# Kernel optimization log

Measured on AMD Instinct MI355X. Metric: run time of the kernel, lower is better.

The kernel has to match this reference:

```python
import jax, jax.numpy as jnp
import numpy as np

B, D, N, K = 16, 128, 16384, 64


def setup_inputs() -> dict:
    key = jax.random.key(0)
    k1, k2, k3, k4 = jax.random.split(key, 4)
    x = jax.random.normal(k1, (B, D, N), dtype=jnp.float32)
    mu = jax.random.normal(k2, (K, D), dtype=jnp.float32)
    log_sigma = 0.1 * jax.random.normal(k3, (K, D), dtype=jnp.float32)
    log_alpha = 0.1 * jax.random.normal(k4, (K,), dtype=jnp.float32)
    return {"x": x, "mu": mu, "log_sigma": log_sigma, "log_alpha": log_alpha}


def reference(x, mu, log_sigma, log_alpha):
    # x: (B, D, N) -> (B, N, D)
    xt = jnp.transpose(x, (0, 2, 1))
    # F.normalize(mu): L2-normalize each cluster center along D (eps=1e-12)
    mu_n = mu / jnp.maximum(jnp.linalg.norm(mu, axis=1, keepdims=True), 1e-12)
    sigma_inv = jnp.exp(-log_sigma)                     # (K, D)
    log_sigma_sum = jnp.sum(log_sigma, axis=1)          # (K,)
    # dist_{bnk} = sum_d (x-mu)^2 * sinv, decomposed into GEMMs
    xsq_term = jnp.einsum('bnd,kd->bnk', xt * xt, sigma_inv)
    cross = jnp.einsum('bnd,kd->bnk', xt, mu_n * sigma_inv)
    mu_term = jnp.sum(mu_n * mu_n * sigma_inv, axis=1)  # (K,)
    dist = xsq_term - 2.0 * cross + mu_term
    logits = -dist + log_alpha - 0.5 * log_sigma_sum    # (B, N, K)
    posterior = jax.nn.softmax(logits, axis=-1)
    return jnp.transpose(posterior, (0, 2, 1))          # (B, K, N)
```

## Files before the change

kernel.cpp:

```cpp
#include <hip/hip_runtime.h>

#define LOG2E 1.4426950408889634f

constexpr int Dn = 128;
constexpr int Nn = 16384;
constexpr int Kn = 64;
constexpr int Bn = 16;

typedef __attribute__((ext_vector_type(16))) float f32x16;

__global__ __launch_bounds__(64) void gmm_prep(const float* __restrict__ mu,
                                               const float* __restrict__ log_sigma,
                                               const float* __restrict__ log_alpha,
                                               float4* __restrict__ wout,
                                               float* __restrict__ cout) {
    const int k = blockIdx.x;
    const int l = threadIdx.x;
    const int d0 = 2 * l;
    float m0 = mu[k * Dn + d0];
    float m1 = mu[k * Dn + d0 + 1];
    float s0 = log_sigma[k * Dn + d0];
    float s1 = log_sigma[k * Dn + d0 + 1];
    float nrm2 = m0 * m0 + m1 * m1;
    float lss = s0 + s1;
    #pragma unroll
    for (int off = 32; off > 0; off >>= 1) {
        nrm2 += __shfl_xor(nrm2, off);
        lss  += __shfl_xor(lss, off);
    }
    const float inv_nrm = 1.0f / fmaxf(sqrtf(nrm2), 1e-12f);
    const float mn0 = m0 * inv_nrm, mn1 = m1 * inv_nrm;
    const float si0 = expf(-s0), si1 = expf(-s1);
    float mt = mn0 * mn0 * si0 + mn1 * mn1 * si1;
    #pragma unroll
    for (int off = 32; off > 0; off >>= 1) mt += __shfl_xor(mt, off);
    wout[((k >> 3) * 64 + l) * 8 + (k & 7)] =
        make_float4(-si0 * LOG2E, 2.0f * mn0 * si0 * LOG2E,
                    -si1 * LOG2E, 2.0f * mn1 * si1 * LOG2E);
    if (l == 0) cout[k] = (log_alpha[k] - 0.5f * lss - mt) * LOG2E;
}

__device__ __forceinline__ float4 fmax4(float4 a, float4 b) {
    return make_float4(fmaxf(a.x, b.x), fmaxf(a.y, b.y),
                       fmaxf(a.z, b.z), fmaxf(a.w, b.w));
}
__device__ __forceinline__ float4 add4(float4 a, float4 b) {
    return make_float4(a.x + b.x, a.y + b.y, a.z + b.z, a.w + b.w);
}

__global__ __launch_bounds__(512)
void gmm_main(const float* __restrict__ x,
              const float4* __restrict__ w,
              const float* __restrict__ cks,
              float* __restrict__ out) {
    __shared__ float sRed[8][256];

    const int tid = threadIdx.x;
    const int g = __builtin_amdgcn_readfirstlane(tid >> 6);
    const int l = tid & 63;
    const int b = blockIdx.y;
    const int nloc = 4 * l;
    const size_t nbase = (size_t)blockIdx.x * 256 + nloc;

    float acc[8][4];
    #pragma unroll
    for (int k = 0; k < 8; ++k) {
        const float c = cks[g * 8 + k];
        #pragma unroll
        for (int j = 0; j < 4; ++j) acc[k][j] = c;
    }

    const float* xp = x + (size_t)b * Dn * Nn + nbase;
    const char* wp = (const char*)w + (size_t)g * 8192;

    #pragma unroll 1
    for (int dh = 0; dh < Dn / 2; ++dh) {
        const float4 xa = *(const float4*)(xp);
        const float4 xb = *(const float4*)(xp + Nn);
        xp += 2 * Nn;

        f32x16 w0, w1;
        asm("s_load_dwordx16 %0, %2, 0x0\n\t"
            "s_load_dwordx16 %1, %2, 0x40\n\t"
            "s_waitcnt lgkmcnt(0)"
            : "=&s"(w0), "=&s"(w1)
            : "s"(wp));
        wp += 128;

        const float4 ta = make_float4(xa.x * xa.x, xa.y * xa.y,
                                      xa.z * xa.z, xa.w * xa.w);
        const float4 tb = make_float4(xb.x * xb.x, xb.y * xb.y,
                                      xb.z * xb.z, xb.w * xb.w);

#define GMM_K(WV, KK, A)                                                  \
        {                                                                 \
            const float wx0 = WV[4 * KK + 0], wy0 = WV[4 * KK + 1];       \
            const float wx1 = WV[4 * KK + 2], wy1 = WV[4 * KK + 3];       \
            A[0] = fmaf(wx0, ta.x, A[0]); A[0] = fmaf(wy0, xa.x, A[0]);   \
            A[0] = fmaf(wx1, tb.x, A[0]); A[0] = fmaf(wy1, xb.x, A[0]);   \
            A[1] = fmaf(wx0, ta.y, A[1]); A[1] = fmaf(wy0, xa.y, A[1]);   \
            A[1] = fmaf(wx1, tb.y, A[1]); A[1] = fmaf(wy1, xb.y, A[1]);   \
            A[2] = fmaf(wx0, ta.z, A[2]); A[2] = fmaf(wy0, xa.z, A[2]);   \
            A[2] = fmaf(wx1, tb.z, A[2]); A[2] = fmaf(wy1, xb.z, A[2]);   \
            A[3] = fmaf(wx0, ta.w, A[3]); A[3] = fmaf(wy0, xa.w, A[3]);   \
            A[3] = fmaf(wx1, tb.w, A[3]); A[3] = fmaf(wy1, xb.w, A[3]);   \
        }

        GMM_K(w0, 0, acc[0]); GMM_K(w0, 1, acc[1]);
        GMM_K(w0, 2, acc[2]); GMM_K(w0, 3, acc[3]);
        GMM_K(w1, 0, acc[4]); GMM_K(w1, 1, acc[5]);
        GMM_K(w1, 2, acc[6]); GMM_K(w1, 3, acc[7]);
#undef GMM_K
    }

    float4 m = make_float4(acc[0][0], acc[0][1], acc[0][2], acc[0][3]);
    #pragma unroll
    for (int k = 1; k < 8; ++k)
        m = fmax4(m, make_float4(acc[k][0], acc[k][1], acc[k][2], acc[k][3]));
    *(float4*)&sRed[g][nloc] = m;
    __syncthreads();
    #pragma unroll
    for (int gg = 0; gg < 8; ++gg)
        m = fmax4(m, *(const float4*)&sRed[gg][nloc]);
    __syncthreads();

    float4 s = make_float4(0.f, 0.f, 0.f, 0.f);
    #pragma unroll
    for (int k = 0; k < 8; ++k) {
        acc[k][0] = __builtin_amdgcn_exp2f(acc[k][0] - m.x); s.x += acc[k][0];
        acc[k][1] = __builtin_amdgcn_exp2f(acc[k][1] - m.y); s.y += acc[k][1];
        acc[k][2] = __builtin_amdgcn_exp2f(acc[k][2] - m.z); s.z += acc[k][2];
        acc[k][3] = __builtin_amdgcn_exp2f(acc[k][3] - m.w); s.w += acc[k][3];
    }
    *(float4*)&sRed[g][nloc] = s;
    __syncthreads();
    s = make_float4(0.f, 0.f, 0.f, 0.f);
    #pragma unroll
    for (int gg = 0; gg < 8; ++gg)
        s = add4(s, *(const float4*)&sRed[gg][nloc]);
    const float4 r = make_float4(1.0f / s.x, 1.0f / s.y, 1.0f / s.z, 1.0f / s.w);

    float* op = out + (size_t)(b * Kn + g * 8) * Nn + nbase;
    #pragma unroll
    for (int k = 0; k < 8; ++k) {
        *(float4*)op = make_float4(acc[k][0] * r.x, acc[k][1] * r.y,
                                   acc[k][2] * r.z, acc[k][3] * r.w);
        op += Nn;
    }
}

extern "C" void kernel_launch(void* const* d_in, const int* in_sizes, int n_in,
                              void* d_out, int out_size, void* d_ws, size_t ws_size,
                              hipStream_t stream) {
    const float* x  = (const float*)d_in[0];
    const float* mu = (const float*)d_in[1];
    const float* ls = (const float*)d_in[2];
    const float* la = (const float*)d_in[3];
    float* out = (float*)d_out;

    float4* wbuf = (float4*)d_ws;
    float*  cbuf = (float*)((char*)d_ws + (size_t)Kn * (Dn / 2) * sizeof(float4));

    gmm_prep<<<dim3(Kn), dim3(64), 0, stream>>>(mu, ls, la, wbuf, cbuf);
    gmm_main<<<dim3(Nn / 256, Bn), dim3(512), 0, stream>>>(x, wbuf, cbuf, out);
}
```

Measured before the change: 261.5 us.

## Compute GMM distance GEMMs with split-bf16 MFMA instead of scalar FMA

Replaces the per-thread FP32 FMA loop with v_mfma_f32_16x16x32_bf16. Weights and activations are split into hi/lo bf16 pairs to emulate near-FP32 accuracy, using three MFMAs per product term. The prep kernel now writes weights in MFMA fragment layout. The main kernel stages converted x tiles in LDS and uses smaller 64-column blocks with a cross-wave softmax reduction. The goal is to move the compute-bound inner product onto matrix cores, at the cost of bf16-split conversion work, scalar (non-vectorized) output stores and some accuracy risk.

```diff
diff --git a/kernel.cpp b/kernel.cpp
--- a/kernel.cpp
+++ b/kernel.cpp
@@ -7,12 +7,18 @@
 constexpr int Kn = 64;
 constexpr int Bn = 16;
 
-typedef __attribute__((ext_vector_type(16))) float f32x16;
+typedef float f32x4 __attribute__((ext_vector_type(4)));
+typedef unsigned int u32x4 __attribute__((ext_vector_type(4)));
+
+__device__ __forceinline__ unsigned int rnhi(float f) {
+    unsigned int u = __float_as_uint(f);
+    return (u + 0x7FFFu + ((u >> 16) & 1u)) & 0xFFFF0000u;
+}
 
 __global__ __launch_bounds__(64) void gmm_prep(const float* __restrict__ mu,
                                                const float* __restrict__ log_sigma,
                                                const float* __restrict__ log_alpha,
-                                               float4* __restrict__ wout,
+                                               unsigned short* __restrict__ wfrag,
                                                float* __restrict__ cout) {
     const int k = blockIdx.x;
     const int l = threadIdx.x;
@@ -34,118 +40,169 @@
     float mt = mn0 * mn0 * si0 + mn1 * mn1 * si1;
     #pragma unroll
     for (int off = 32; off > 0; off >>= 1) mt += __shfl_xor(mt, off);
-    wout[((k >> 3) * 64 + l) * 8 + (k & 7)] =
-        make_float4(-si0 * LOG2E, 2.0f * mn0 * si0 * LOG2E,
-                    -si1 * LOG2E, 2.0f * mn1 * si1 * LOG2E);
+
+    const float av[2] = {-si0 * LOG2E, -si1 * LOG2E};
+    const float bv[2] = {2.0f * mn0 * si0 * LOG2E, 2.0f * mn1 * si1 * LOG2E};
+    const int ks = k >> 4;
+    #pragma unroll
+    for (int dd = 0; dd < 2; ++dd) {
+        const int d = d0 + dd;
+        const unsigned int ah = rnhi(av[dd]);
+        const unsigned int al = rnhi(av[dd] - __uint_as_float(ah));
+        const unsigned int bh = rnhi(bv[dd]);
+        const unsigned int bl = rnhi(bv[dd] - __uint_as_float(bh));
+        const int s = d >> 5, h = (d >> 3) & 3, j = d & 7;
+        const int lane = (h << 4) | (k & 15);
+        const size_t base = ((size_t)((ks * 4 + s) * 4) * 64 + lane) * 8 + j;
+        wfrag[base + 0 * 64 * 8] = (unsigned short)(ah >> 16);
+        wfrag[base + 1 * 64 * 8] = (unsigned short)(al >> 16);
+        wfrag[base + 2 * 64 * 8] = (unsigned short)(bh >> 16);
+        wfrag[base + 3 * 64 * 8] = (unsigned short)(bl >> 16);
+    }
     if (l == 0) cout[k] = (log_alpha[k] - 0.5f * lss - mt) * LOG2E;
 }
 
-__device__ __forceinline__ float4 fmax4(float4 a, float4 b) {
-    return make_float4(fmaxf(a.x, b.x), fmaxf(a.y, b.y),
-                       fmaxf(a.z, b.z), fmaxf(a.w, b.w));
-}
-__device__ __forceinline__ float4 add4(float4 a, float4 b) {
-    return make_float4(a.x + b.x, a.y + b.y, a.z + b.z, a.w + b.w);
-}
-
 __global__ __launch_bounds__(512)
+__attribute__((amdgpu_waves_per_eu(4, 4)))
 void gmm_main(const float* __restrict__ x,
-              const float4* __restrict__ w,
+              const unsigned short* __restrict__ wf,
               const float* __restrict__ cks,
               float* __restrict__ out) {
-    __shared__ float sRed[8][256];
+    __shared__ unsigned short sB[4][4][4][64][8];
+    __shared__ float sRedM[4][64];
+    __shared__ float sRedS[4][64];
 
     const int tid = threadIdx.x;
-    const int g = __builtin_amdgcn_readfirstlane(tid >> 6);
     const int l = tid & 63;
     const int b = blockIdx.y;
-    const int nloc = 4 * l;
-    const size_t nbase = (size_t)blockIdx.x * 256 + nloc;
-
-    float acc[8][4];
-    #pragma unroll
-    for (int k = 0; k < 8; ++k) {
-        const float c = cks[g * 8 + k];
-        #pragma unroll
-        for (int j = 0; j < 4; ++j) acc[k][j] = c;
-    }
-
-    const float* xp = x + (size_t)b * Dn * Nn + nbase;
-    const char* wp = (const char*)w + (size_t)g * 8192;
-
-    #pragma unroll 1
-    for (int dh = 0; dh < Dn / 2; ++dh) {
-        const float4 xa = *(const float4*)(xp);
-        const float4 xb = *(const float4*)(xp + Nn);
-        xp += 2 * Nn;
-
-        f32x16 w0, w1;
-        asm("s_load_dwordx16 %0, %2, 0x0\n\t"
-            "s_load_dwordx16 %1, %2, 0x40\n\t"
-            "s_waitcnt lgkmcnt(0)"
-            : "=&s"(w0), "=&s"(w1)
-            : "s"(wp));
-        wp += 128;
-
-        const float4 ta = make_float4(xa.x * xa.x, xa.y * xa.y,
-                                      xa.z * xa.z, xa.w * xa.w);
-        const float4 tb = make_float4(xb.x * xb.x, xb.y * xb.y,
-                                      xb.z * xb.z, xb.w * xb.w);
-
-#define GMM_K(WV, KK, A)                                                  \
-        {                                                                 \
-            const float wx0 = WV[4 * KK + 0], wy0 = WV[4 * KK + 1];       \
-            const float wx1 = WV[4 * KK + 2], wy1 = WV[4 * KK + 3];       \
-            A[0] = fmaf(wx0, ta.x, A[0]); A[0] = fmaf(wy0, xa.x, A[0]);   \
-            A[0] = fmaf(wx1, tb.x, A[0]); A[0] = fmaf(wy1, xb.x, A[0]);   \
-            A[1] = fmaf(wx0, ta.y, A[1]); A[1] = fmaf(wy0, xa.y, A[1]);   \
-            A[1] = fmaf(wx1, tb.y, A[1]); A[1] = fmaf(wy1, xb.y, A[1]);   \
-            A[2] = fmaf(wx0, ta.z, A[2]); A[2] = fmaf(wy0, xa.z, A[2]);   \
-            A[2] = fmaf(wx1, tb.z, A[2]); A[2] = fmaf(wy1, xb.z, A[2]);   \
-            A[3] = fmaf(wx0, ta.w, A[3]); A[3] = fmaf(wy0, xa.w, A[3]);   \
-            A[3] = fmaf(wx1, tb.w, A[3]); A[3] = fmaf(wy1, xb.w, A[3]);   \
-        }
-
-        GMM_K(w0, 0, acc[0]); GMM_K(w0, 1, acc[1]);
-        GMM_K(w0, 2, acc[2]); GMM_K(w0, 3, acc[3]);
-        GMM_K(w1, 0, acc[4]); GMM_K(w1, 1, acc[5]);
-        GMM_K(w1, 2, acc[6]); GMM_K(w1, 3, acc[7]);
-#undef GMM_K
-    }
-
-    float4 m = make_float4(acc[0][0], acc[0][1], acc[0][2], acc[0][3]);
-    #pragma unroll
-    for (int k = 1; k < 8; ++k)
-        m = fmax4(m, make_float4(acc[k][0], acc[k][1], acc[k][2], acc[k][3]));
-    *(float4*)&sRed[g][nloc] = m;
+    const int nwin = blockIdx.x * 64;
+    const float* xwin = x + (size_t)b * Dn * Nn + nwin;
+
+    float xv[2][8];
+    #pragma unroll
+    for (int i = 0; i < 2; ++i) {
+        const int o = (tid >> 6) + 8 * i;
+        #pragma unroll
+        for (int jj = 0; jj < 8; ++jj)
+            xv[i][jj] = xwin[(size_t)(o * 8 + jj) * Nn + l];
+    }
+    #pragma unroll
+    for (int i = 0; i < 2; ++i) {
+        const int o = (tid >> 6) + 8 * i;
+        const int s = o >> 2, h = o & 3;
+        const int lane = (h << 4) | (l & 15), tt = l >> 4;
+        unsigned int XH[4], XL[4], TH[4], TL[4];
+        #pragma unroll
+        for (int p = 0; p < 4; ++p) {
+            const float x0 = xv[i][2 * p], x1 = xv[i][2 * p + 1];
+            const float t0 = x0 * x0, t1 = x1 * x1;
+            const unsigned int xh0 = rnhi(x0), xh1 = rnhi(x1);
+            const unsigned int xq0 = rnhi(x0 - __uint_as_float(xh0));
+            const unsigned int xq1 = rnhi(x1 - __uint_as_float(xh1));
+            const unsigned int th0 = rnhi(t0), th1 = rnhi(t1);
+            const unsigned int tq0 = rnhi(t0 - __uint_as_float(th0));
+            const unsigned int tq1 = rnhi(t1 - __uint_as_float(th1));
+            XH[p] = (xh0 >> 16) | xh1;
+            XL[p] = (xq0 >> 16) | xq1;
+            TH[p] = (th0 >> 16) | th1;
+            TL[p] = (tq0 >> 16) | tq1;
+        }
+        *(u32x4*)&sB[0][s][tt][lane][0] = u32x4{XH[0], XH[1], XH[2], XH[3]};
+        *(u32x4*)&sB[1][s][tt][lane][0] = u32x4{XL[0], XL[1], XL[2], XL[3]};
+        *(u32x4*)&sB[2][s][tt][lane][0] = u32x4{TH[0], TH[1], TH[2], TH[3]};
+        *(u32x4*)&sB[3][s][tt][lane][0] = u32x4{TL[0], TL[1], TL[2], TL[3]};
+    }
+
+    const int wid = __builtin_amdgcn_readfirstlane(tid >> 6);
+    const int ks = wid & 3, tp = wid >> 2;
+    u32x4 W[4][4];
+    #pragma unroll
+    for (int s = 0; s < 4; ++s)
+        #pragma unroll
+        for (int m = 0; m < 4; ++m)
+            W[s][m] = *(const u32x4*)(wf + ((size_t)((ks * 4 + s) * 4 + m) * 64 + l) * 8);
+
+    f32x4 acc[2];
+    #pragma unroll
+    for (int tt = 0; tt < 2; ++tt)
+        #pragma unroll
+        for (int r = 0; r < 4; ++r)
+            acc[tt][r] = cks[ks * 16 + (l >> 4) * 4 + r];
+
     __syncthreads();
-    #pragma unroll
-    for (int gg = 0; gg < 8; ++gg)
-        m = fmax4(m, *(const float4*)&sRed[gg][nloc]);
+
+#define MFMA(C, A, B_) asm("v_mfma_f32_16x16x32_bf16 %0, %1, %2, %0" \
+                           : "+v"(C) : "v"(A), "v"(B_))
+    asm volatile("s_nop 1");
+    #pragma unroll
+    for (int s = 0; s < 4; ++s) {
+        #pragma unroll
+        for (int tt = 0; tt < 2; ++tt) {
+            const int ttg = tp * 2 + tt;
+            const u32x4 Xh = *(const u32x4*)&sB[0][s][ttg][l][0];
+            const u32x4 Xl = *(const u32x4*)&sB[1][s][ttg][l][0];
+            const u32x4 Th = *(const u32x4*)&sB[2][s][ttg][l][0];
+            const u32x4 Tl = *(const u32x4*)&sB[3][s][ttg][l][0];
+            MFMA(acc[tt], W[s][0], Th);
+            MFMA(acc[tt], W[s][1], Th);
+            MFMA(acc[tt], W[s][0], Tl);
+            MFMA(acc[tt], W[s][2], Xh);
+            MFMA(acc[tt], W[s][3], Xh);
+            MFMA(acc[tt], W[s][2], Xl);
+        }
+    }
+#undef MFMA
+    asm volatile("s_nop 7\n\ts_nop 7");
+
+    float mw[2];
+    #pragma unroll
+    for (int tt = 0; tt < 2; ++tt) {
+        float m = fmaxf(fmaxf(acc[tt][0], acc[tt][1]),
+                        fmaxf(acc[tt][2], acc[tt][3]));
+        m = fmaxf(m, __shfl_xor(m, 16));
+        m = fmaxf(m, __shfl_xor(m, 32));
+        mw[tt] = m;
+        if (l < 16) sRedM[ks][(tp * 2 + tt) * 16 + l] = m;
+    }
     __syncthreads();
-
-    float4 s = make_float4(0.f, 0.f, 0.f, 0.f);
-    #pragma unroll
-    for (int k = 0; k < 8; ++k) {
-        acc[k][0] = __builtin_amdgcn_exp2f(acc[k][0] - m.x); s.x += acc[k][0];
-        acc[k][1] = __builtin_amdgcn_exp2f(acc[k][1] - m.y); s.y += acc[k][1];
-        acc[k][2] = __builtin_amdgcn_exp2f(acc[k][2] - m.z); s.z += acc[k][2];
-        acc[k][3] = __builtin_amdgcn_exp2f(acc[k][3] - m.w); s.w += acc[k][3];
-    }
-    *(float4*)&sRed[g][nloc] = s;
+    float M[2], stot[2];
+    #pragma unroll
+    for (int tt = 0; tt < 2; ++tt) {
+        const int ttg = tp * 2 + tt;
+        float m = sRedM[0][ttg * 16 + (l & 15)];
+        m = fmaxf(m, sRedM[1][ttg * 16 + (l & 15)]);
+        m = fmaxf(m, sRedM[2][ttg * 16 + (l & 15)]);
+        m = fmaxf(m, sRedM[3][ttg * 16 + (l & 15)]);
+        M[tt] = m;
+        float ssum = 0.f;
+        #pragma unroll
+        for (int r = 0; r < 4; ++r) {
+            acc[tt][r] = __builtin_amdgcn_exp2f(acc[tt][r] - m);
+            ssum += acc[tt][r];
+        }
+        ssum += __shfl_xor(ssum, 16);
+        ssum += __shfl_xor(ssum, 32);
+        if (l < 16) sRedS[ks][ttg * 16 + l] = ssum;
+    }
     __syncthreads();
-    s = make_float4(0.f, 0.f, 0.f, 0.f);
-    #pragma unroll
-    for (int gg = 0; gg < 8; ++gg)
-        s = add4(s, *(const float4*)&sRed[gg][nloc]);
-    const float4 r = make_float4(1.0f / s.x, 1.0f / s.y, 1.0f / s.z, 1.0f / s.w);
-
-    float* op = out + (size_t)(b * Kn + g * 8) * Nn + nbase;
-    #pragma unroll
-    for (int k = 0; k < 8; ++k) {
-        *(float4*)op = make_float4(acc[k][0] * r.x, acc[k][1] * r.y,
-                                   acc[k][2] * r.z, acc[k][3] * r.w);
-        op += Nn;
+    #pragma unroll
+    for (int tt = 0; tt < 2; ++tt) {
+        const int ttg = tp * 2 + tt;
+        stot[tt] = sRedS[0][ttg * 16 + (l & 15)] + sRedS[1][ttg * 16 + (l & 15)] +
+                   sRedS[2][ttg * 16 + (l & 15)] + sRedS[3][ttg * 16 + (l & 15)];
+    }
+
+    #pragma unroll
+    for (int tt = 0; tt < 2; ++tt) {
+        const int ttg = tp * 2 + tt;
+        const float inv = 1.0f / stot[tt];
+        float* op = out + ((size_t)(b * Kn + ks * 16 + (l >> 4) * 4)) * Nn +
+                    nwin + ttg * 16 + (l & 15);
+        #pragma unroll
+        for (int r = 0; r < 4; ++r) {
+            *op = acc[tt][r] * inv;
+            op += Nn;
+        }
     }
 }
 
@@ -158,9 +215,9 @@
     const float* la = (const float*)d_in[3];
     float* out = (float*)d_out;
 
-    float4* wbuf = (float4*)d_ws;
-    float*  cbuf = (float*)((char*)d_ws + (size_t)Kn * (Dn / 2) * sizeof(float4));
+    unsigned short* wbuf = (unsigned short*)d_ws;
+    float* cbuf = (float*)((char*)d_ws + 65536);
 
     gmm_prep<<<dim3(Kn), dim3(64), 0, stream>>>(mu, ls, la, wbuf, cbuf);
-    gmm_main<<<dim3(Nn / 256, Bn), dim3(512), 0, stream>>>(x, wbuf, cbuf, out);
-}
+    gmm_main<<<dim3(Nn / 64, Bn), dim3(512), 0, stream>>>(x, wbuf, cbuf, out);
+}
```

Result: faster. 221.9 us (-15.2%).
